# Performance work log

Measured on AMD Instinct MI355X. Metric: run time of the kernel, lower is better.

Reference implementation:

```python
import jax, jax.numpy as jnp
import numpy as np

HIDDEN_DIM = 256  # scale = sqrt(hidden_dim); D = 2*hidden_dim because is_bi_rnn=True
B, L, D = 4, 4096, 512


def setup_inputs() -> dict:
    key = jax.random.key(0)
    k1, k2, k3, k4, k5 = jax.random.split(key, 5)
    inputs = jax.random.normal(k1, (B, L, D), dtype=jnp.float32)
    # torch nn.Linear(D, D, bias=False) weights, applied as x @ W.T
    Wq = jax.random.normal(k2, (D, D), dtype=jnp.float32) / np.float32(np.sqrt(D))
    Wk = jax.random.normal(k3, (D, D), dtype=jnp.float32) / np.float32(np.sqrt(D))
    Wv = jax.random.normal(k4, (D, D), dtype=jnp.float32) / np.float32(np.sqrt(D))
    # valid lengths per batch element; max must equal L (source uses maxlen = max(lens))
    lens = jax.random.randint(k5, (B,), L // 2, L + 1).at[0].set(L)
    return {"inputs": inputs, "Wq": Wq, "Wk": Wk, "Wv": Wv, "lens": lens}


def reference(inputs, Wq, Wk, Wv, lens):
    # QKV projections (torch Linear: x @ W.T)
    Q = inputs @ Wq.T            # [B, L, D]
    K = inputs @ Wk.T            # [B, L, D]
    V = inputs @ Wv.T            # [B, L, D]
    scale = jnp.asarray(HIDDEN_DIM, inputs.dtype) ** 0.5
    scores = jnp.einsum('bqd,bkd->bqk', Q, K) / scale  # [B, L, L]
    # FAITHFUL: F.softmax with no dim on a 3-D tensor -> legacy torch dim=0 (batch axis)
    W = jax.nn.softmax(scores, axis=0)
    # post-softmax mask over QUERY rows: mask[b, q] = q < lens[b]
    mask = (jnp.arange(L)[None, :] < lens[:, None]).astype(W.dtype)  # [B, L]
    W = W * mask[:, :, None]
    Z = jnp.einsum('bqk,bkd->bqd', W, V)   # [B, L, D]
    return jnp.sum(Z, axis=1, keepdims=True)  # [B, 1, D]
```

## Files before the change

### kernel.cpp

```cpp
#include <hip/hip_runtime.h>

#define BB 4
#define LL 4096
#define DD 512

typedef __attribute__((ext_vector_type(8))) short bf16x8;
typedef __attribute__((ext_vector_type(4))) float f32x4;
typedef __attribute__((ext_vector_type(4))) unsigned short ushort4v;

__device__ __forceinline__ unsigned short bf16_rne(float x) {
    unsigned u = __float_as_uint(x);
    unsigned r = (u + 0x7FFFu + ((u >> 16) & 1u)) >> 16;
    return (unsigned short)r;
}

__global__ __launch_bounds__(256) void split_x(const float* __restrict__ X,
                                               unsigned short* __restrict__ Xh,
                                               unsigned short* __restrict__ Xl) {
    const size_t i = ((size_t)blockIdx.x * 256 + threadIdx.x) * 4;
    float4 x4 = *reinterpret_cast<const float4*>(X + i);
    float v[4] = {x4.x, x4.y, x4.z, x4.w};
    ushort4v h4, l4;
    #pragma unroll
    for (int j = 0; j < 4; ++j) {
        unsigned short h = bf16_rne(v[j]);
        float lo = v[j] - __uint_as_float((unsigned)h << 16);
        h4[j] = h;
        l4[j] = bf16_rne(lo);
    }
    *reinterpret_cast<ushort4v*>(Xh + i) = h4;
    *reinterpret_cast<ushort4v*>(Xl + i) = l4;
}

__global__ __launch_bounds__(256) void gemm_tn_M(const float* __restrict__ A,
                                                 const float* __restrict__ B,
                                                 unsigned short* __restrict__ Mh,
                                                 unsigned short* __restrict__ Ml,
                                                 float scale) {
    __shared__ float As[16][68];
    __shared__ float Bs[16][68];
    const int tid = threadIdx.x;
    const int tx = tid & 15, ty = tid >> 4;
    const int iBase = blockIdx.x * 64;
    const int jBase = blockIdx.y * 64;
    const int dr = tid >> 4;
    const int c4 = (tid & 15) << 2;

    float acc[4][4] = {};
    for (int d0 = 0; d0 < DD; d0 += 16) {
        float4 a4 = *reinterpret_cast<const float4*>(A + (size_t)(d0 + dr) * DD + iBase + c4);
        float4 b4 = *reinterpret_cast<const float4*>(B + (size_t)(d0 + dr) * DD + jBase + c4);
        __syncthreads();
        *reinterpret_cast<float4*>(&As[dr][c4]) = a4;
        *reinterpret_cast<float4*>(&Bs[dr][c4]) = b4;
        __syncthreads();
        #pragma unroll
        for (int t = 0; t < 16; ++t) {
            float4 q4 = *reinterpret_cast<const float4*>(&As[t][ty << 2]);
            float4 k4 = *reinterpret_cast<const float4*>(&Bs[t][tx << 2]);
            float q[4] = {q4.x, q4.y, q4.z, q4.w};
            float k[4] = {k4.x, k4.y, k4.z, k4.w};
            #pragma unroll
            for (int i = 0; i < 4; ++i)
                #pragma unroll
                for (int j = 0; j < 4; ++j)
                    acc[i][j] = fmaf(q[i], k[j], acc[i][j]);
        }
    }
    #pragma unroll
    for (int i = 0; i < 4; ++i)
        #pragma unroll
        for (int j = 0; j < 4; ++j) {
            float v = acc[i][j] * scale;
            unsigned short h = bf16_rne(v);
            float lo = v - __uint_as_float((unsigned)h << 16);
            size_t off = (size_t)(iBase + (ty << 2) + i) * DD + jBase + (tx << 2) + j;
            Mh[off] = h;
            Ml[off] = bf16_rne(lo);
        }
}

#define GLOAD_LDS16(SRC, DST)                                                  \
    __builtin_amdgcn_global_load_lds(                                          \
        (const __attribute__((address_space(1))) void*)(SRC),                  \
        (__attribute__((address_space(3))) void*)(DST), 16, 0, 0)

__device__ __forceinline__ void stage8(const unsigned short* __restrict__ g,
                                       unsigned short* l) {
    const int ln = threadIdx.x & 63;
    const int r = ln >> 3;
    const int c = ln & 7;
    const unsigned short* src = g + (size_t)r * DD + ((c ^ r) << 3);
    GLOAD_LDS16(src, l);
}

__device__ __forceinline__ bf16x8 ldfrag(const unsigned short* base, int row16,
                                         int kk) {
    const int lane = threadIdx.x & 63;
    const int r = row16 + (lane & 15);
    const int boff = r * 128 + ((((kk + ((lane >> 4) << 3)) << 1)) ^ ((r & 7) << 4));
    return *reinterpret_cast<const bf16x8*>(
        reinterpret_cast<const char*>(base) + boff);
}

__global__ __launch_bounds__(256, 3) void gemm_nt_T(
    const unsigned short* __restrict__ Xh_g, const unsigned short* __restrict__ Xl_g,
    const unsigned short* __restrict__ Mh_g, const unsigned short* __restrict__ Ml_g,
    unsigned short* __restrict__ Th_g, unsigned short* __restrict__ Tl_g) {
    __shared__ unsigned short Ah_s[128][64];
    __shared__ unsigned short Al_s[128][64];
    __shared__ unsigned short Bh_s[64][64];
    __shared__ unsigned short Bl_s[64][64];

    const int rBase = blockIdx.x * 128;
    const int cBase = blockIdx.y * 64;
    const int w = threadIdx.x >> 6;
    const int lane = threadIdx.x & 63;
    const int wq = (w >> 1) * 64;
    const int wk = (w & 1) * 32;

    f32x4 acc[4][2] = {};

    for (int dcc = 0; dcc < 8; ++dcc) {
        const int dc = dcc << 6;
        __syncthreads();
        #pragma unroll
        for (int s = 0; s < 4; ++s) {
            const int r0 = w * 32 + s * 8;
            stage8(Xh_g + (size_t)(rBase + r0) * DD + dc, &Ah_s[r0][0]);
            stage8(Xl_g + (size_t)(rBase + r0) * DD + dc, &Al_s[r0][0]);
        }
        #pragma unroll
        for (int s = 0; s < 2; ++s) {
            const int r0 = w * 16 + s * 8;
            stage8(Mh_g + (size_t)(cBase + r0) * DD + dc, &Bh_s[r0][0]);
            stage8(Ml_g + (size_t)(cBase + r0) * DD + dc, &Bl_s[r0][0]);
        }
        __syncthreads();
        #pragma unroll
        for (int kk = 0; kk < 64; kk += 32) {
            bf16x8 bh0 = ldfrag(&Bh_s[0][0], wk + 0, kk);
            bf16x8 bh1 = ldfrag(&Bh_s[0][0], wk + 16, kk);
            bf16x8 bl0 = ldfrag(&Bl_s[0][0], wk + 0, kk);
            bf16x8 bl1 = ldfrag(&Bl_s[0][0], wk + 16, kk);
            #pragma unroll
            for (int i = 0; i < 4; ++i) {
                bf16x8 ah = ldfrag(&Ah_s[0][0], wq + i * 16, kk);
                bf16x8 al = ldfrag(&Al_s[0][0], wq + i * 16, kk);
                acc[i][0] = __builtin_amdgcn_mfma_f32_16x16x32_bf16(ah, bh0, acc[i][0], 0, 0, 0);
                acc[i][0] = __builtin_amdgcn_mfma_f32_16x16x32_bf16(ah, bl0, acc[i][0], 0, 0, 0);
                acc[i][0] = __builtin_amdgcn_mfma_f32_16x16x32_bf16(al, bh0, acc[i][0], 0, 0, 0);
                acc[i][1] = __builtin_amdgcn_mfma_f32_16x16x32_bf16(ah, bh1, acc[i][1], 0, 0, 0);
                acc[i][1] = __builtin_amdgcn_mfma_f32_16x16x32_bf16(ah, bl1, acc[i][1], 0, 0, 0);
                acc[i][1] = __builtin_amdgcn_mfma_f32_16x16x32_bf16(al, bh1, acc[i][1], 0, 0, 0);
            }
        }
    }

    #pragma unroll
    for (int i = 0; i < 4; ++i)
        #pragma unroll
        for (int r = 0; r < 4; ++r) {
            const int row = rBase + wq + i * 16 + ((lane >> 4) << 2) + r;
            #pragma unroll
            for (int j = 0; j < 2; ++j) {
                const int col = cBase + wk + j * 16 + (lane & 15);
                float v = acc[i][j][r];
                unsigned short h = bf16_rne(v);
                float lo = v - __uint_as_float((unsigned)h << 16);
                Th_g[(size_t)row * DD + col] = h;
                Tl_g[(size_t)row * DD + col] = bf16_rne(lo);
            }
        }
}

__global__ __launch_bounds__(256, 3) void scores_wsum(
    const unsigned short* __restrict__ Qh_g, const unsigned short* __restrict__ Ql_g,
    const unsigned short* __restrict__ Kh_g, const unsigned short* __restrict__ Kl_g,
    const int* __restrict__ lens, float* __restrict__ wsum) {
    __shared__ unsigned short Qh_s[128][64];
    __shared__ unsigned short Ql_s[128][64];
    __shared__ unsigned short Kh_s[64][64];
    __shared__ unsigned short Kl_s[64][64];

    const int qBase = blockIdx.x * 128;
    const int kBase = blockIdx.y * 64;
    const int w = threadIdx.x >> 6;
    const int lane = threadIdx.x & 63;
    const int wq = (w >> 1) * 64;
    const int wk = (w & 1) * 32;

    const int l0 = lens[0], l1 = lens[1], l2 = lens[2], l3 = lens[3];

    f32x4 acc[4][4][2] = {};

    #pragma unroll
    for (int b = 0; b < BB; ++b) {
        const unsigned short* qh = Qh_g + (size_t)(b * LL + qBase) * DD;
        const unsigned short* ql = Ql_g + (size_t)(b * LL + qBase) * DD;
        const unsigned short* kh = Kh_g + (size_t)(b * LL + kBase) * DD;
        const unsigned short* kl = Kl_g + (size_t)(b * LL + kBase) * DD;
        for (int dcc = 0; dcc < 8; ++dcc) {
            const int dc = dcc << 6;
            __syncthreads();
            #pragma unroll
            for (int s = 0; s < 4; ++s) {
                const int r0 = w * 32 + s * 8;
                stage8(qh + (size_t)r0 * DD + dc, &Qh_s[r0][0]);
                stage8(ql + (size_t)r0 * DD + dc, &Ql_s[r0][0]);
            }
            #pragma unroll
            for (int s = 0; s < 2; ++s) {
                const int r0 = w * 16 + s * 8;
                stage8(kh + (size_t)r0 * DD + dc, &Kh_s[r0][0]);
                stage8(kl + (size_t)r0 * DD + dc, &Kl_s[r0][0]);
            }
            __syncthreads();
            #pragma unroll
            for (int kk = 0; kk < 64; kk += 32) {
                bf16x8 bh0 = ldfrag(&Kh_s[0][0], wk + 0, kk);
                bf16x8 bh1 = ldfrag(&Kh_s[0][0], wk + 16, kk);
                bf16x8 bl0 = ldfrag(&Kl_s[0][0], wk + 0, kk);
                bf16x8 bl1 = ldfrag(&Kl_s[0][0], wk + 16, kk);
                #pragma unroll
                for (int i = 0; i < 4; ++i) {
                    bf16x8 ah = ldfrag(&Qh_s[0][0], wq + i * 16, kk);
                    bf16x8 al = ldfrag(&Ql_s[0][0], wq + i * 16, kk);
                    acc[b][i][0] = __builtin_amdgcn_mfma_f32_16x16x32_bf16(ah, bh0, acc[b][i][0], 0, 0, 0);
                    acc[b][i][0] = __builtin_amdgcn_mfma_f32_16x16x32_bf16(ah, bl0, acc[b][i][0], 0, 0, 0);
                    acc[b][i][0] = __builtin_amdgcn_mfma_f32_16x16x32_bf16(al, bh0, acc[b][i][0], 0, 0, 0);
                    acc[b][i][1] = __builtin_amdgcn_mfma_f32_16x16x32_bf16(ah, bh1, acc[b][i][1], 0, 0, 0);
                    acc[b][i][1] = __builtin_amdgcn_mfma_f32_16x16x32_bf16(ah, bl1, acc[b][i][1], 0, 0, 0);
                    acc[b][i][1] = __builtin_amdgcn_mfma_f32_16x16x32_bf16(al, bh1, acc[b][i][1], 0, 0, 0);
                }
            }
        }
    }

    float psum[4][2] = {};
    #pragma unroll
    for (int i = 0; i < 4; ++i) {
        #pragma unroll
        for (int r = 0; r < 4; ++r) {
            const int q = qBase + wq + i * 16 + ((lane >> 4) << 2) + r;
            #pragma unroll
            for (int j = 0; j < 2; ++j) {
                float e0 = __expf(acc[0][i][j][r]);
                float e1 = __expf(acc[1][i][j][r]);
                float e2 = __expf(acc[2][i][j][r]);
                float e3 = __expf(acc[3][i][j][r]);
                float inv = 1.0f / (e0 + e1 + e2 + e3);
                psum[0][j] += (q < l0) ? e0 * inv : 0.0f;
                psum[1][j] += (q < l1) ? e1 * inv : 0.0f;
                psum[2][j] += (q < l2) ? e2 * inv : 0.0f;
                psum[3][j] += (q < l3) ? e3 * inv : 0.0f;
            }
        }
    }
    #pragma unroll
    for (int bb = 0; bb < 4; ++bb)
        #pragma unroll
        for (int j = 0; j < 2; ++j) {
            float v = psum[bb][j];
            v += __shfl_xor(v, 16);
            v += __shfl_xor(v, 32);
            if (lane < 16)
                atomicAdd(&wsum[bb * LL + kBase + wk + j * 16 + lane], v);
        }
}

__global__ __launch_bounds__(256) void wsum_x(const float* __restrict__ X,
                                              const float* __restrict__ wsum,
                                              float* __restrict__ y) {
    const int b = blockIdx.y;
    const int e = blockIdx.x * 256 + threadIdx.x;
    const int kc = blockIdx.z * 64;
    const float* Xp = X + ((size_t)b * LL + kc) * DD + e;
    const float* wp = wsum + b * LL + kc;
    float a = 0.0f;
    #pragma unroll 4
    for (int k = 0; k < 64; ++k) a = fmaf(wp[k], Xp[(size_t)k * DD], a);
    atomicAdd(&y[b * DD + e], a);
}

__global__ __launch_bounds__(256) void y_out(const float* __restrict__ Wv,
                                             const float* __restrict__ y,
                                             float* __restrict__ out) {
    const int b = blockIdx.y;
    const int d = blockIdx.x * 256 + threadIdx.x;
    const float* wv = Wv + (size_t)d * DD;
    const float* yb = y + b * DD;
    float a = 0.0f;
    #pragma unroll 4
    for (int e = 0; e < DD; e += 4) {
        float4 w4 = *reinterpret_cast<const float4*>(wv + e);
        float4 y4 = *reinterpret_cast<const float4*>(yb + e);
        a += w4.x * y4.x + w4.y * y4.y + w4.z * y4.z + w4.w * y4.w;
    }
    out[b * DD + d] = a;
}

extern "C" void kernel_launch(void* const* d_in, const int* in_sizes, int n_in,
                              void* d_out, int out_size, void* d_ws, size_t ws_size,
                              hipStream_t stream) {
    const float* X  = (const float*)d_in[0];
    const float* Wq = (const float*)d_in[1];
    const float* Wk = (const float*)d_in[2];
    const float* Wv = (const float*)d_in[3];
    const int* lens = (const int*)d_in[4];
    float* out = (float*)d_out;

    char* ws = (char*)d_ws;
    unsigned short* Xh  = (unsigned short*)ws;
    unsigned short* Xl  = (unsigned short*)(ws + ((size_t)16 << 20));
    unsigned short* Th  = (unsigned short*)(ws + ((size_t)32 << 20));
    unsigned short* Tl  = (unsigned short*)(ws + ((size_t)48 << 20));
    unsigned short* Mth = (unsigned short*)(ws + ((size_t)64 << 20));
    unsigned short* Mtl = (unsigned short*)(ws + ((size_t)64 << 20) + (512u << 10));
    float* wsum = (float*)(ws + ((size_t)65 << 20));
    float* y    = (float*)(ws + ((size_t)65 << 20) + 65536);

    hipMemsetAsync(wsum, 0,
                   (size_t)BB * LL * sizeof(float) + (size_t)BB * DD * sizeof(float),
                   stream);

    dim3 blk(256);
    split_x<<<dim3(8192), blk, 0, stream>>>(X, Xh, Xl);
    gemm_tn_M<<<dim3(8, 8), blk, 0, stream>>>(Wk, Wq, Mth, Mtl, 0.0625f);
    gemm_nt_T<<<dim3(128, 8), blk, 0, stream>>>(Xh, Xl, Mth, Mtl, Th, Tl);
    scores_wsum<<<dim3(32, 64), blk, 0, stream>>>(Th, Tl, Xh, Xl, lens, wsum);
    wsum_x<<<dim3(2, 4, 64), blk, 0, stream>>>(X, wsum, y);
    y_out<<<dim3(2, 4), blk, 0, stream>>>(Wv, y, out);
}
```

Measured before the change: 374.9 us.

## Double-buffer scores kernel LDS with interleaved hi/lo tiles and prefetch

```diff
diff --git a/kernel.cpp b/kernel.cpp
--- a/kernel.cpp
+++ b/kernel.cpp
@@ -103,6 +103,28 @@
         reinterpret_cast<const char*>(base) + boff);
 }
 
+__device__ __forceinline__ void stage8_hl(const unsigned short* __restrict__ gh,
+                                          const unsigned short* __restrict__ gl,
+                                          unsigned short* dst) {
+    const int ln = threadIdx.x & 63;
+    const int r = ln >> 3;
+    const int p = ln & 7;
+    const int e = p ^ r;
+    const unsigned short* g = (e < 4) ? gh : gl;
+    const unsigned short* src = g + (size_t)r * DD + ((e & 3) << 3);
+    GLOAD_LDS16(src, dst);
+}
+
+__device__ __forceinline__ bf16x8 ldfrag32(const unsigned short* base, int row16,
+                                           int low) {
+    const int lane = threadIdx.x & 63;
+    const int r = row16 + (lane & 15);
+    const int e = (lane >> 4) + (low << 2);
+    const int boff = (r << 7) + ((e << 4) ^ ((r & 7) << 4));
+    return *reinterpret_cast<const bf16x8*>(
+        reinterpret_cast<const char*>(base) + boff);
+}
+
 __global__ __launch_bounds__(256, 3) void gemm_nt_T(
     const unsigned short* __restrict__ Xh_g, const unsigned short* __restrict__ Xl_g,
     const unsigned short* __restrict__ Mh_g, const unsigned short* __restrict__ Ml_g,
@@ -175,13 +197,11 @@
 }
 
 __global__ __launch_bounds__(256, 3) void scores_wsum(
-    const unsigned short* __restrict__ Qh_g, const unsigned short* __restrict__ Ql_g,
-    const unsigned short* __restrict__ Kh_g, const unsigned short* __restrict__ Kl_g,
+    const unsigned short* __restrict__ Th_g, const unsigned short* __restrict__ Tl_g,
+    const unsigned short* __restrict__ Xh_g, const unsigned short* __restrict__ Xl_g,
     const int* __restrict__ lens, float* __restrict__ wsum) {
-    __shared__ unsigned short Qh_s[128][64];
-    __shared__ unsigned short Ql_s[128][64];
-    __shared__ unsigned short Kh_s[64][64];
-    __shared__ unsigned short Kl_s[64][64];
+    __shared__ unsigned short TT[2][128][64];
+    __shared__ unsigned short XX[2][64][64];
 
     const int qBase = blockIdx.x * 128;
     const int kBase = blockIdx.y * 64;
@@ -194,46 +214,54 @@
 
     f32x4 acc[4][4][2] = {};
 
-    #pragma unroll
-    for (int b = 0; b < BB; ++b) {
-        const unsigned short* qh = Qh_g + (size_t)(b * LL + qBase) * DD;
-        const unsigned short* ql = Ql_g + (size_t)(b * LL + qBase) * DD;
-        const unsigned short* kh = Kh_g + (size_t)(b * LL + kBase) * DD;
-        const unsigned short* kl = Kl_g + (size_t)(b * LL + kBase) * DD;
-        for (int dcc = 0; dcc < 8; ++dcc) {
-            const int dc = dcc << 6;
-            __syncthreads();
-            #pragma unroll
-            for (int s = 0; s < 4; ++s) {
-                const int r0 = w * 32 + s * 8;
-                stage8(qh + (size_t)r0 * DD + dc, &Qh_s[r0][0]);
-                stage8(ql + (size_t)r0 * DD + dc, &Ql_s[r0][0]);
-            }
-            #pragma unroll
-            for (int s = 0; s < 2; ++s) {
-                const int r0 = w * 16 + s * 8;
-                stage8(kh + (size_t)r0 * DD + dc, &Kh_s[r0][0]);
-                stage8(kl + (size_t)r0 * DD + dc, &Kl_s[r0][0]);
+    auto stage = [&](int tn) {
+        const int bn = tn >> 4;
+        const int dcn = (tn & 15) << 5;
+        const unsigned short* th = Th_g + ((size_t)(bn * LL + qBase)) * DD + dcn;
+        const unsigned short* tl = Tl_g + ((size_t)(bn * LL + qBase)) * DD + dcn;
+        const unsigned short* xh = Xh_g + ((size_t)(bn * LL + kBase)) * DD + dcn;
+        const unsigned short* xl = Xl_g + ((size_t)(bn * LL + kBase)) * DD + dcn;
+        const int cb = tn & 1;
+        #pragma unroll
+        for (int s = 0; s < 4; ++s) {
+            const int r0 = w * 32 + s * 8;
+            stage8_hl(th + (size_t)r0 * DD, tl + (size_t)r0 * DD, &TT[cb][r0][0]);
+        }
+        #pragma unroll
+        for (int s = 0; s < 2; ++s) {
+            const int r0 = w * 16 + s * 8;
+            stage8_hl(xh + (size_t)r0 * DD, xl + (size_t)r0 * DD, &XX[cb][r0][0]);
+        }
+    };
+
+    stage(0);
+    __syncthreads();
+
+    #pragma unroll
+    for (int b = 0; b < 4; ++b) {
+        #pragma unroll
+        for (int d = 0; d < 16; ++d) {
+            const int t = b * 16 + d;
+            if (t < 63) stage(t + 1);
+            const int cb = t & 1;
+            const unsigned short* Tb = &TT[cb][0][0];
+            const unsigned short* Xb = &XX[cb][0][0];
+            bf16x8 bh0 = ldfrag32(Xb, wk + 0, 0);
+            bf16x8 bh1 = ldfrag32(Xb, wk + 16, 0);
+            bf16x8 bl0 = ldfrag32(Xb, wk + 0, 1);
+            bf16x8 bl1 = ldfrag32(Xb, wk + 16, 1);
+            #pragma unroll
+            for (int i = 0; i < 4; ++i) {
+                bf16x8 ah = ldfrag32(Tb, wq + i * 16, 0);
+                bf16x8 al = ldfrag32(Tb, wq + i * 16, 1);
+                acc[b][i][0] = __builtin_amdgcn_mfma_f32_16x16x32_bf16(ah, bh0, acc[b][i][0], 0, 0, 0);
+                acc[b][i][0] = __builtin_amdgcn_mfma_f32_16x16x32_bf16(ah, bl0, acc[b][i][0], 0, 0, 0);
+                acc[b][i][0] = __builtin_amdgcn_mfma_f32_16x16x32_bf16(al, bh0, acc[b][i][0], 0, 0, 0);
+                acc[b][i][1] = __builtin_amdgcn_mfma_f32_16x16x32_bf16(ah, bh1, acc[b][i][1], 0, 0, 0);
+                acc[b][i][1] = __builtin_amdgcn_mfma_f32_16x16x32_bf16(ah, bl1, acc[b][i][1], 0, 0, 0);
+                acc[b][i][1] = __builtin_amdgcn_mfma_f32_16x16x32_bf16(al, bh1, acc[b][i][1], 0, 0, 0);
             }
             __syncthreads();
-            #pragma unroll
-            for (int kk = 0; kk < 64; kk += 32) {
-                bf16x8 bh0 = ldfrag(&Kh_s[0][0], wk + 0, kk);
-                bf16x8 bh1 = ldfrag(&Kh_s[0][0], wk + 16, kk);
-                bf16x8 bl0 = ldfrag(&Kl_s[0][0], wk + 0, kk);
-                bf16x8 bl1 = ldfrag(&Kl_s[0][0], wk + 16, kk);
-                #pragma unroll
-                for (int i = 0; i < 4; ++i) {
-                    bf16x8 ah = ldfrag(&Qh_s[0][0], wq + i * 16, kk);
-                    bf16x8 al = ldfrag(&Ql_s[0][0], wq + i * 16, kk);
-                    acc[b][i][0] = __builtin_amdgcn_mfma_f32_16x16x32_bf16(ah, bh0, acc[b][i][0], 0, 0, 0);
-                    acc[b][i][0] = __builtin_amdgcn_mfma_f32_16x16x32_bf16(ah, bl0, acc[b][i][0], 0, 0, 0);
-                    acc[b][i][0] = __builtin_amdgcn_mfma_f32_16x16x32_bf16(al, bh0, acc[b][i][0], 0, 0, 0);
-                    acc[b][i][1] = __builtin_amdgcn_mfma_f32_16x16x32_bf16(ah, bh1, acc[b][i][1], 0, 0, 0);
-                    acc[b][i][1] = __builtin_amdgcn_mfma_f32_16x16x32_bf16(ah, bl1, acc[b][i][1], 0, 0, 0);
-                    acc[b][i][1] = __builtin_amdgcn_mfma_f32_16x16x32_bf16(al, bh1, acc[b][i][1], 0, 0, 0);
-                }
-            }
         }
     }
 
```

Result: slower. 409.6 us (+9.2%).

## Remap workgroups per XCD for L2 locality and stage GEMM epilogue through LDS

Applied to the files above, without the earlier changes.

```diff
diff --git a/kernel.cpp b/kernel.cpp
--- a/kernel.cpp
+++ b/kernel.cpp
@@ -7,6 +7,7 @@
 typedef __attribute__((ext_vector_type(8))) short bf16x8;
 typedef __attribute__((ext_vector_type(4))) float f32x4;
 typedef __attribute__((ext_vector_type(4))) unsigned short ushort4v;
+typedef __attribute__((ext_vector_type(4))) unsigned int u32x4;
 
 __device__ __forceinline__ unsigned short bf16_rne(float x) {
     unsigned u = __float_as_uint(x);
@@ -112,8 +113,11 @@
     __shared__ unsigned short Bh_s[64][64];
     __shared__ unsigned short Bl_s[64][64];
 
-    const int rBase = blockIdx.x * 128;
-    const int cBase = blockIdx.y * 64;
+    const int lin = blockIdx.x;
+    const int wgid = ((lin & 7) << 7) + (lin >> 3);
+    const int rBase = (wgid >> 3) * 128;
+    const int cBase = (wgid & 7) * 64;
+
     const int w = threadIdx.x >> 6;
     const int lane = threadIdx.x & 63;
     const int wq = (w >> 1) * 64;
@@ -157,21 +161,39 @@
         }
     }
 
+    __syncthreads();
+    char* hB = reinterpret_cast<char*>(&Ah_s[0][0]);
+    char* lB = reinterpret_cast<char*>(&Al_s[0][0]);
     #pragma unroll
     for (int i = 0; i < 4; ++i)
         #pragma unroll
         for (int r = 0; r < 4; ++r) {
-            const int row = rBase + wq + i * 16 + ((lane >> 4) << 2) + r;
+            const int row = wq + i * 16 + ((lane >> 4) << 2) + r;
             #pragma unroll
             for (int j = 0; j < 2; ++j) {
-                const int col = cBase + wk + j * 16 + (lane & 15);
+                const int col = wk + j * 16 + (lane & 15);
                 float v = acc[i][j][r];
                 unsigned short h = bf16_rne(v);
                 float lo = v - __uint_as_float((unsigned)h << 16);
-                Th_g[(size_t)row * DD + col] = h;
-                Tl_g[(size_t)row * DD + col] = bf16_rne(lo);
-            }
-        }
+                const int bo = (row << 7) + (((col << 1)) ^ ((row & 7) << 4));
+                *reinterpret_cast<unsigned short*>(hB + bo) = h;
+                *reinterpret_cast<unsigned short*>(lB + bo) = bf16_rne(lo);
+            }
+        }
+    __syncthreads();
+    const int tid = threadIdx.x;
+    #pragma unroll
+    for (int s = 0; s < 4; ++s) {
+        const int slot = s * 256 + tid;
+        const int row = slot >> 3;
+        const int sl = slot & 7;
+        const int bo = (row << 7) + (((sl << 4)) ^ ((row & 7) << 4));
+        u32x4 hv = *reinterpret_cast<const u32x4*>(hB + bo);
+        u32x4 lv = *reinterpret_cast<const u32x4*>(lB + bo);
+        const size_t go = (size_t)(rBase + row) * DD + cBase + (sl << 3);
+        *reinterpret_cast<u32x4*>(Th_g + go) = hv;
+        *reinterpret_cast<u32x4*>(Tl_g + go) = lv;
+    }
 }
 
 __global__ __launch_bounds__(256, 3) void scores_wsum(
@@ -183,8 +205,13 @@
     __shared__ unsigned short Kh_s[64][64];
     __shared__ unsigned short Kl_s[64][64];
 
-    const int qBase = blockIdx.x * 128;
-    const int kBase = blockIdx.y * 64;
+    const int lin = blockIdx.x;
+    const int wgid = ((lin & 7) << 8) + (lin >> 3);
+    const int sub = wgid & 255;
+    const int xcd = wgid >> 8;
+    const int qBase = (((xcd & 1) << 4) + (sub & 15)) * 128;
+    const int kBase = (((xcd >> 1) << 4) + (sub >> 4)) * 64;
+
     const int w = threadIdx.x >> 6;
     const int lane = threadIdx.x & 63;
     const int wq = (w >> 1) * 64;
@@ -327,8 +354,8 @@
     dim3 blk(256);
     split_x<<<dim3(8192), blk, 0, stream>>>(X, Xh, Xl);
     gemm_tn_M<<<dim3(8, 8), blk, 0, stream>>>(Wk, Wq, Mth, Mtl, 0.0625f);
-    gemm_nt_T<<<dim3(128, 8), blk, 0, stream>>>(Xh, Xl, Mth, Mtl, Th, Tl);
-    scores_wsum<<<dim3(32, 64), blk, 0, stream>>>(Th, Tl, Xh, Xl, lens, wsum);
+    gemm_nt_T<<<dim3(1024), blk, 0, stream>>>(Xh, Xl, Mth, Mtl, Th, Tl);
+    scores_wsum<<<dim3(2048), blk, 0, stream>>>(Th, Tl, Xh, Xl, lens, wsum);
     wsum_x<<<dim3(2, 4, 64), blk, 0, stream>>>(X, wsum, y);
     y_out<<<dim3(2, 4), blk, 0, stream>>>(Wv, y, out);
 }
```

Measured after the change: 366.6 us. -2.2%, faster.
